# Kernel optimization log

Measured on AMD Instinct MI355X. Metric: run time of the kernel, lower is better.

Reference implementation:

```python
import jax, jax.numpy as jnp
import numpy as np

N_NODES = 50000
N_EDGES = 1200000
IN_DIM = 128
EDGE_DIM = 64
EMBED_DIM = 64
NUM_HEADS = 8


def segment_softmax(logits, segment_ids, num_segments):
    # numerically stable softmax over segments (receivers)
    mx = jax.ops.segment_max(logits, segment_ids, num_segments)
    e = jnp.exp(logits - mx[segment_ids])
    denom = jax.ops.segment_sum(e, segment_ids, num_segments)
    return e / denom[segment_ids]


def mish(x):
    return x * jnp.tanh(jax.nn.softplus(x))


def setup_inputs() -> dict:
    key = jax.random.key(0)
    ks = jax.random.split(key, 8)
    node_features = jax.random.normal(ks[0], (N_NODES, IN_DIM), dtype=jnp.float32)
    edge_features = jax.random.normal(ks[1], (N_EDGES, EDGE_DIM), dtype=jnp.float32)
    global_features = jax.random.normal(ks[2], (32,), dtype=jnp.float32)
    senders = jax.random.randint(ks[3], (N_EDGES,), 0, N_NODES, dtype=jnp.int32)
    receivers = jax.random.randint(ks[4], (N_EDGES,), 0, N_NODES, dtype=jnp.int32)
    W_kernel = jax.random.normal(ks[5], (IN_DIM, EMBED_DIM), dtype=jnp.float32) * (2.0 / (IN_DIM + EMBED_DIM)) ** 0.5
    W_bias = jnp.zeros((EMBED_DIM,), dtype=jnp.float32)
    We_kernel = jax.random.normal(ks[6], (EDGE_DIM, EMBED_DIM), dtype=jnp.float32) * (2.0 / (EDGE_DIM + EMBED_DIM)) ** 0.5
    We_bias = jnp.zeros((EMBED_DIM,), dtype=jnp.float32)
    a = jax.random.normal(ks[7], (NUM_HEADS, EMBED_DIM // NUM_HEADS), dtype=jnp.float32) * (2.0 / (NUM_HEADS + EMBED_DIM // NUM_HEADS)) ** 0.5
    return dict(node_features=node_features, edge_features=edge_features,
                global_features=global_features, senders=senders, receivers=receivers,
                W_kernel=W_kernel, W_bias=W_bias, We_kernel=We_kernel, We_bias=We_bias, a=a)


def reference(node_features, edge_features, global_features, senders, receivers,
              W_kernel, W_bias, We_kernel, We_bias, a):
    num_nodes = node_features.shape[0]
    H, D = a.shape  # num_heads, head_dim
    # share_weights=True: one Dense projects nodes for both send and recv roles
    nodes = node_features @ W_kernel + W_bias            # [N, H*D]
    send_edges = nodes[senders]                          # [E, H*D] gather
    recv_edges = nodes[receivers]                        # [E, H*D] gather
    x = send_edges + recv_edges + (edge_features @ We_kernel + We_bias)
    x = mish(x)
    xh = x.reshape(-1, H, D)                             # [E, H, D]
    attn_logits = jnp.sum(xh * a, axis=-1, keepdims=True)  # [E, H, 1]
    attn_weights = segment_softmax(attn_logits, receivers, num_nodes)  # [E, H, 1]
    edges = attn_weights * send_edges.reshape(-1, H, D)  # [E, H, D]
    edges = edges.reshape(-1, H * D)
    new_nodes = jax.ops.segment_sum(edges, receivers, num_nodes)  # [N, H*D]
    return new_nodes
```

## Files before the change

kernel.cpp:

```cpp
#include <hip/hip_runtime.h>
#include <math.h>

#define IN_DIM   128
#define EDGE_DIM 64
#define ED       64
#define NH       8
#define CAP      64

typedef __attribute__((ext_vector_type(8))) __bf16 bf16x8;
typedef __attribute__((ext_vector_type(4))) __bf16 bf16x4;
typedef __attribute__((ext_vector_type(4))) float  f32x4;

__device__ __forceinline__ int atomInc(int* p) {
    return __hip_atomic_fetch_add(p, 1, __ATOMIC_RELAXED, __HIP_MEMORY_SCOPE_AGENT);
}

__device__ __forceinline__ float mish_f(float x) {
    float u  = __expf(fminf(x, 15.f));
    float nn = u * (u + 2.f);
    return x * __fdividef(nn, nn + 2.f);
}

__global__ __launch_bounds__(256) void bucket_k(const int* __restrict__ rcv,
                         const int* __restrict__ snd,
                         int* __restrict__ deg, int2* __restrict__ buck, int nE) {
    for (int i = blockIdx.x * 256 + threadIdx.x; i < nE; i += gridDim.x * 256) {
        int r = rcv[i];
        int slot = atomInc(&deg[r]);
        if (slot < CAP) buck[(long)r * CAP + slot] = make_int2(i, snd[i]);
    }
}

__global__ __launch_bounds__(256) void node_proj(const float* __restrict__ nf,
                          const float* __restrict__ W,
                          const float* __restrict__ Wb,
                          __bf16* __restrict__ nodes_bf, int nN) {
    int lane = threadIdx.x & 63;
    int col  = lane & 15;
    int q    = lane >> 4;
    int wid    = blockIdx.x * (blockDim.x >> 6) + (threadIdx.x >> 6);
    int nwaves = gridDim.x * (blockDim.x >> 6);

    bf16x8 aw[4][4];
#pragma unroll
    for (int c = 0; c < 4; c++)
#pragma unroll
        for (int s = 0; s < 4; s++)
#pragma unroll
            for (int i = 0; i < 8; i++)
                aw[c][s][i] = (__bf16)W[(s * 32 + q * 8 + i) * ED + c * 16 + col];
    f32x4 wbv[4];
#pragma unroll
    for (int c = 0; c < 4; c++)
#pragma unroll
        for (int r = 0; r < 4; r++)
            wbv[c][r] = Wb[c * 16 + q * 4 + r];

    int ngroups = (nN + 15) >> 4;
    for (int g = wid; g < ngroups; g += nwaves) {
        int n = g * 16 + col;
        bool valid = (n < nN);
        long nb = (long)(valid ? n : nN - 1) * IN_DIM;
        bf16x8 bfr[4];
#pragma unroll
        for (int s = 0; s < 4; s++) {
            float4 f0 = *(const float4*)(nf + nb + s * 32 + q * 8);
            float4 f1 = *(const float4*)(nf + nb + s * 32 + q * 8 + 4);
            bfr[s][0] = (__bf16)f0.x; bfr[s][1] = (__bf16)f0.y;
            bfr[s][2] = (__bf16)f0.z; bfr[s][3] = (__bf16)f0.w;
            bfr[s][4] = (__bf16)f1.x; bfr[s][5] = (__bf16)f1.y;
            bfr[s][6] = (__bf16)f1.z; bfr[s][7] = (__bf16)f1.w;
        }
        f32x4 acc[4];
#pragma unroll
        for (int c = 0; c < 4; c++) {
            acc[c] = wbv[c];
#pragma unroll
            for (int s = 0; s < 4; s++)
                acc[c] = __builtin_amdgcn_mfma_f32_16x16x32_bf16(aw[c][s], bfr[s], acc[c], 0, 0, 0);
        }
        if (valid) {
#pragma unroll
            for (int c = 0; c < 4; c++) {
                bf16x4 b;
#pragma unroll
                for (int r = 0; r < 4; r++) b[r] = (__bf16)acc[c][r];
                *(bf16x4*)(nodes_bf + (long)n * ED + c * 16 + q * 4) = b;
            }
        }
    }
}

__global__ __launch_bounds__(256) void gemm_pass1(
                           const float* __restrict__ ef,
                           const int* __restrict__ snd,
                           const int* __restrict__ rcv,
                           const __bf16* __restrict__ nodes_bf,
                           const float* __restrict__ We,
                           const float* __restrict__ Web,
                           const float* __restrict__ a,
                           __bf16* __restrict__ w8, int nE) {
    int lane = threadIdx.x & 63;
    int col  = lane & 15;
    int q    = lane >> 4;
    int wid    = blockIdx.x * (blockDim.x >> 6) + (threadIdx.x >> 6);
    int nwaves = gridDim.x * (blockDim.x >> 6);

    bf16x8 aw[4][2];
#pragma unroll
    for (int c = 0; c < 4; c++)
#pragma unroll
        for (int s = 0; s < 2; s++)
#pragma unroll
            for (int i = 0; i < 8; i++)
                aw[c][s][i] = (__bf16)We[(s * 32 + q * 8 + i) * ED + c * 16 + col];
    f32x4 wbv[4];
    float ahat[4][4];
#pragma unroll
    for (int c = 0; c < 4; c++)
#pragma unroll
        for (int r = 0; r < 4; r++) {
            int j = c * 16 + q * 4 + r;
            wbv[c][r]  = Web[j];
            ahat[c][r] = a[j];
        }

    int ngroups = (nE + 15) >> 4;
    for (int g = wid; g < ngroups; g += nwaves) {
        int e = g * 16 + col;
        bool valid = (e < nE);
        int ec = valid ? e : nE - 1;
        long eb = (long)ec * EDGE_DIM;
        bf16x8 bfr[2];
#pragma unroll
        for (int s = 0; s < 2; s++) {
            f32x4 f0 = __builtin_nontemporal_load((const f32x4*)(ef + eb + s * 32 + q * 8));
            f32x4 f1 = __builtin_nontemporal_load((const f32x4*)(ef + eb + s * 32 + q * 8 + 4));
            bfr[s][0] = (__bf16)f0[0]; bfr[s][1] = (__bf16)f0[1];
            bfr[s][2] = (__bf16)f0[2]; bfr[s][3] = (__bf16)f0[3];
            bfr[s][4] = (__bf16)f1[0]; bfr[s][5] = (__bf16)f1[1];
            bfr[s][6] = (__bf16)f1[2]; bfr[s][7] = (__bf16)f1[3];
        }
        f32x4 acc[4];
#pragma unroll
        for (int c = 0; c < 4; c++) {
            acc[c] = wbv[c];
            acc[c] = __builtin_amdgcn_mfma_f32_16x16x32_bf16(aw[c][0], bfr[0], acc[c], 0, 0, 0);
            acc[c] = __builtin_amdgcn_mfma_f32_16x16x32_bf16(aw[c][1], bfr[1], acc[c], 0, 0, 0);
        }
        int se = snd[ec], re = rcv[ec];
        float p[4];
#pragma unroll
        for (int c = 0; c < 4; c++) {
            int j0 = c * 16 + q * 4;
            bf16x4 svb = *(const bf16x4*)(nodes_bf + (long)se * ED + j0);
            bf16x4 rvb = *(const bf16x4*)(nodes_bf + (long)re * ED + j0);
            float ph = 0.f;
#pragma unroll
            for (int r = 0; r < 4; r++) {
                float x = acc[c][r] + (float)svb[r] + (float)rvb[r];
                ph = fmaf(mish_f(x), ahat[c][r], ph);
            }
            p[c] = ph;
        }
        float w[4];
#pragma unroll
        for (int c = 0; c < 4; c++) {
            p[c] += __shfl_xor(p[c], 16);
            w[c] = __expf(p[c]);
        }
        if (valid) {
            if (q == 0) {
                bf16x4 v;
#pragma unroll
                for (int c = 0; c < 4; c++) v[c] = (__bf16)w[c];
                *(bf16x4*)(w8 + (long)e * NH) = v;
            } else if (q == 2) {
                bf16x4 v;
#pragma unroll
                for (int c = 0; c < 4; c++) v[c] = (__bf16)w[c];
                *(bf16x4*)(w8 + (long)e * NH + 4) = v;
            }
        }
    }
}

__global__ __launch_bounds__(256) void seg_sum(const int* __restrict__ deg,
                        const int2* __restrict__ buck,
                        const __bf16* __restrict__ w8,
                        const __bf16* __restrict__ nodes_bf,
                        float* __restrict__ out, int nN) {
    int rn = blockIdx.x * 4 + (threadIdx.x >> 6);
    if (rn >= nN) return;
    int j = threadIdx.x & 63;
    int h = j >> 3;
    int widx = (h & 1) * 4 + (h >> 1);
    int dg = min(deg[rn], CAP);
    long base = (long)rn * CAP;
    float acc = 0.f, dn = 0.f;
#pragma unroll 2
    for (int s = 0; s < dg; s++) {
        int2 be = buck[base + s];
        float w  = (float)w8[(long)be.x * NH + widx];
        float sv = (float)nodes_bf[(long)be.y * ED + j];
        acc = fmaf(w, sv, acc);
        dn += w;
    }
    out[(long)rn * ED + j] = (dn > 0.f) ? __fdividef(acc, dn) : 0.f;
}

extern "C" void kernel_launch(void* const* d_in, const int* in_sizes, int n_in,
                              void* d_out, int out_size, void* d_ws, size_t ws_size,
                              hipStream_t stream) {
    const float* nf  = (const float*)d_in[0];
    const float* ef  = (const float*)d_in[1];
    const int*   snd = (const int*)d_in[3];
    const int*   rcv = (const int*)d_in[4];
    const float* W   = (const float*)d_in[5];
    const float* Wb  = (const float*)d_in[6];
    const float* We  = (const float*)d_in[7];
    const float* Web = (const float*)d_in[8];
    const float* a   = (const float*)d_in[9];

    int nN = in_sizes[0] / IN_DIM;
    int nE = in_sizes[3];
    float* out = (float*)d_out;

    __bf16* nodes_bf = (__bf16*)d_ws;
    __bf16* w8       = nodes_bf + (size_t)nN * ED;
    int*    deg      = (int*)(w8 + (size_t)nE * NH);
    int2*   buck     = (int2*)(deg + nN);

    hipMemsetAsync(deg, 0, (size_t)nN * sizeof(int), stream);

    bucket_k<<<2048, 256, 0, stream>>>(rcv, snd, deg, buck, nE);
    node_proj<<<512, 256, 0, stream>>>(nf, W, Wb, nodes_bf, nN);
    gemm_pass1<<<2048, 256, 0, stream>>>(ef, snd, rcv, nodes_bf, We, Web, a,
                                         w8, nE);
    seg_sum<<<(nN + 3) / 4, 256, 0, stream>>>(deg, buck, w8, nodes_bf, out, nN);
}
```

Measured before the change: 300.2 us.

## Merge bucketing and node projection into one launch, permute node layout for 16B gathers

```diff
diff --git a/kernel.cpp b/kernel.cpp
--- a/kernel.cpp
+++ b/kernel.cpp
@@ -6,6 +6,7 @@
 #define ED       64
 #define NH       8
 #define CAP      64
+#define NPB      512
 
 typedef __attribute__((ext_vector_type(8))) __bf16 bf16x8;
 typedef __attribute__((ext_vector_type(4))) __bf16 bf16x4;
@@ -21,25 +22,31 @@
     return x * __fdividef(nn, nn + 2.f);
 }
 
-__global__ __launch_bounds__(256) void bucket_k(const int* __restrict__ rcv,
-                         const int* __restrict__ snd,
-                         int* __restrict__ deg, int2* __restrict__ buck, int nE) {
-    for (int i = blockIdx.x * 256 + threadIdx.x; i < nE; i += gridDim.x * 256) {
-        int r = rcv[i];
-        int slot = atomInc(&deg[r]);
-        if (slot < CAP) buck[(long)r * CAP + slot] = make_int2(i, snd[i]);
-    }
-}
-
-__global__ __launch_bounds__(256) void node_proj(const float* __restrict__ nf,
-                          const float* __restrict__ W,
-                          const float* __restrict__ Wb,
-                          __bf16* __restrict__ nodes_bf, int nN) {
+
+__global__ __launch_bounds__(256) void front_k(const float* __restrict__ nf,
+                        const float* __restrict__ W,
+                        const float* __restrict__ Wb,
+                        __bf16* __restrict__ nodes_pf,
+                        const int* __restrict__ rcv,
+                        const int* __restrict__ snd,
+                        int* __restrict__ deg,
+                        int2* __restrict__ buck,
+                        int nN, int nE, int nbk) {
+    if (blockIdx.x >= NPB) {
+        int i0 = (blockIdx.x - NPB) * 256 + threadIdx.x;
+        int stride = nbk * 256;
+        for (int i = i0; i < nE; i += stride) {
+            int r = rcv[i];
+            int slot = atomInc(&deg[r]);
+            if (slot < CAP) buck[(long)r * CAP + slot] = make_int2(i, snd[i]);
+        }
+        return;
+    }
     int lane = threadIdx.x & 63;
     int col  = lane & 15;
     int q    = lane >> 4;
-    int wid    = blockIdx.x * (blockDim.x >> 6) + (threadIdx.x >> 6);
-    int nwaves = gridDim.x * (blockDim.x >> 6);
+    int wid    = blockIdx.x * 4 + (threadIdx.x >> 6);
+    int nwaves = NPB * 4;
 
     bf16x8 aw[4][4];
 #pragma unroll
@@ -80,13 +87,14 @@
                 acc[c] = __builtin_amdgcn_mfma_f32_16x16x32_bf16(aw[c][s], bfr[s], acc[c], 0, 0, 0);
         }
         if (valid) {
-#pragma unroll
-            for (int c = 0; c < 4; c++) {
-                bf16x4 b;
-#pragma unroll
-                for (int r = 0; r < 4; r++) b[r] = (__bf16)acc[c][r];
-                *(bf16x4*)(nodes_bf + (long)n * ED + c * 16 + q * 4) = b;
+            bf16x8 v01, v23;
+#pragma unroll
+            for (int i = 0; i < 8; i++) {
+                v01[i] = (__bf16)acc[i >> 2][i & 3];
+                v23[i] = (__bf16)acc[2 + (i >> 2)][i & 3];
             }
+            *(bf16x8*)(nodes_pf + (long)n * ED + q * 16)     = v01;
+            *(bf16x8*)(nodes_pf + (long)n * ED + q * 16 + 8) = v23;
         }
     }
 }
@@ -95,7 +103,7 @@
                            const float* __restrict__ ef,
                            const int* __restrict__ snd,
                            const int* __restrict__ rcv,
-                           const __bf16* __restrict__ nodes_bf,
+                           const __bf16* __restrict__ nodes_pf,
                            const float* __restrict__ We,
                            const float* __restrict__ Web,
                            const float* __restrict__ a,
@@ -141,6 +149,12 @@
             bfr[s][4] = (__bf16)f1[0]; bfr[s][5] = (__bf16)f1[1];
             bfr[s][6] = (__bf16)f1[2]; bfr[s][7] = (__bf16)f1[3];
         }
+        int se = snd[ec], re = rcv[ec];
+        bf16x8 s01 = *(const bf16x8*)(nodes_pf + (long)se * ED + q * 16);
+        bf16x8 s23 = *(const bf16x8*)(nodes_pf + (long)se * ED + q * 16 + 8);
+        bf16x8 r01 = *(const bf16x8*)(nodes_pf + (long)re * ED + q * 16);
+        bf16x8 r23 = *(const bf16x8*)(nodes_pf + (long)re * ED + q * 16 + 8);
+
         f32x4 acc[4];
 #pragma unroll
         for (int c = 0; c < 4; c++) {
@@ -148,17 +162,15 @@
             acc[c] = __builtin_amdgcn_mfma_f32_16x16x32_bf16(aw[c][0], bfr[0], acc[c], 0, 0, 0);
             acc[c] = __builtin_amdgcn_mfma_f32_16x16x32_bf16(aw[c][1], bfr[1], acc[c], 0, 0, 0);
         }
-        int se = snd[ec], re = rcv[ec];
         float p[4];
 #pragma unroll
         for (int c = 0; c < 4; c++) {
-            int j0 = c * 16 + q * 4;
-            bf16x4 svb = *(const bf16x4*)(nodes_bf + (long)se * ED + j0);
-            bf16x4 rvb = *(const bf16x4*)(nodes_bf + (long)re * ED + j0);
             float ph = 0.f;
 #pragma unroll
             for (int r = 0; r < 4; r++) {
-                float x = acc[c][r] + (float)svb[r] + (float)rvb[r];
+                float sv = (c < 2) ? (float)s01[c * 4 + r] : (float)s23[(c - 2) * 4 + r];
+                float rv = (c < 2) ? (float)r01[c * 4 + r] : (float)r23[(c - 2) * 4 + r];
+                float x = acc[c][r] + sv + rv;
                 ph = fmaf(mish_f(x), ahat[c][r], ph);
             }
             p[c] = ph;
@@ -188,25 +200,37 @@
 __global__ __launch_bounds__(256) void seg_sum(const int* __restrict__ deg,
                         const int2* __restrict__ buck,
                         const __bf16* __restrict__ w8,
-                        const __bf16* __restrict__ nodes_bf,
+                        const __bf16* __restrict__ nodes_pf,
                         float* __restrict__ out, int nN) {
     int rn = blockIdx.x * 4 + (threadIdx.x >> 6);
     if (rn >= nN) return;
     int j = threadIdx.x & 63;
-    int h = j >> 3;
+    int qq = j >> 4, cc = (j >> 2) & 3, rr = j & 3;
+    int f = cc * 16 + qq * 4 + rr;
+    int h = f >> 3;
     int widx = (h & 1) * 4 + (h >> 1);
     int dg = min(deg[rn], CAP);
     long base = (long)rn * CAP;
     float acc = 0.f, dn = 0.f;
-#pragma unroll 2
-    for (int s = 0; s < dg; s++) {
-        int2 be = buck[base + s];
-        float w  = (float)w8[(long)be.x * NH + widx];
-        float sv = (float)nodes_bf[(long)be.y * ED + j];
-        acc = fmaf(w, sv, acc);
-        dn += w;
-    }
-    out[(long)rn * ED + j] = (dn > 0.f) ? __fdividef(acc, dn) : 0.f;
+    for (int s0 = 0; s0 < dg; s0 += 4) {
+        int2 b[4];
+#pragma unroll
+        for (int k = 0; k < 4; k++)
+            b[k] = buck[base + min(s0 + k, dg - 1)];
+        float wv[4], sv[4];
+#pragma unroll
+        for (int k = 0; k < 4; k++) {
+            bool v = (s0 + k) < dg;
+            wv[k] = v ? (float)w8[(long)b[k].x * NH + widx] : 0.f;
+            sv[k] = (float)nodes_pf[(long)b[k].y * ED + j];
+        }
+#pragma unroll
+        for (int k = 0; k < 4; k++) {
+            acc = fmaf(wv[k], sv[k], acc);
+            dn += wv[k];
+        }
+    }
+    out[(long)rn * ED + f] = (dn > 0.f) ? __fdividef(acc, dn) : 0.f;
 }
 
 extern "C" void kernel_launch(void* const* d_in, const int* in_sizes, int n_in,
@@ -226,16 +250,17 @@
     int nE = in_sizes[3];
     float* out = (float*)d_out;
 
-    __bf16* nodes_bf = (__bf16*)d_ws;
-    __bf16* w8       = nodes_bf + (size_t)nN * ED;
+    __bf16* nodes_pf = (__bf16*)d_ws;
+    __bf16* w8       = nodes_pf + (size_t)nN * ED;
     int*    deg      = (int*)(w8 + (size_t)nE * NH);
     int2*   buck     = (int2*)(deg + nN);
 
     hipMemsetAsync(deg, 0, (size_t)nN * sizeof(int), stream);
 
-    bucket_k<<<2048, 256, 0, stream>>>(rcv, snd, deg, buck, nE);
-    node_proj<<<512, 256, 0, stream>>>(nf, W, Wb, nodes_bf, nN);
-    gemm_pass1<<<2048, 256, 0, stream>>>(ef, snd, rcv, nodes_bf, We, Web, a,
+    int nbk = 1536;
+    front_k<<<NPB + nbk, 256, 0, stream>>>(nf, W, Wb, nodes_pf,
+                                           rcv, snd, deg, buck, nN, nE, nbk);
+    gemm_pass1<<<2048, 256, 0, stream>>>(ef, snd, rcv, nodes_pf, We, Web, a,
                                          w8, nE);
-    seg_sum<<<(nN + 3) / 4, 256, 0, stream>>>(deg, buck, w8, nodes_bf, out, nN);
-}
+    seg_sum<<<(nN + 3) / 4, 256, 0, stream>>>(deg, buck, w8, nodes_pf, out, nN);
+}
```

After: 294.3 us. -2.0%, faster.
